# Optimization experiments

Hardware: AMD Instinct MI355X
Metric: run time of the kernel (lower is better)

The kernel has to match this reference:

```python
import jax, jax.numpy as jnp
import numpy as np

NUM_HEADS = 2

def mha(q, k, v, w_in, b_in, w_out, b_out):
    # torch nn.MultiheadAttention with batch_first=True, packed in_proj
    E = q.shape[-1]
    Dh = E // NUM_HEADS
    wq, wk, wv = jnp.split(w_in, 3, axis=0)
    bq, bk, bv = jnp.split(b_in, 3, axis=0)
    qh = (q @ wq.T + bq).reshape(q.shape[0], q.shape[1], NUM_HEADS, Dh)
    kh = (k @ wk.T + bk).reshape(k.shape[0], k.shape[1], NUM_HEADS, Dh)
    vh = (v @ wv.T + bv).reshape(v.shape[0], v.shape[1], NUM_HEADS, Dh)
    scores = jnp.einsum('blhd,bmhd->bhlm', qh, kh) / jnp.sqrt(jnp.asarray(Dh, q.dtype))
    attn = jax.nn.softmax(scores, axis=-1)
    ctx = jnp.einsum('bhlm,bmhd->blhd', attn, vh).reshape(q.shape[0], q.shape[1], E)
    return ctx @ w_out.T + b_out


def setup_inputs() -> dict:
    key = jax.random.key(0)
    ks = jax.random.split(key, 10)
    B, S, F, E, H = 16384, 512, 4, 8, 16
    s = 0.3
    return {
        'x': jax.random.normal(ks[0], (B, S, E), jnp.float32),
        'Q': jax.random.normal(ks[1], (F, E), jnp.float32) * s,
        'sa_w_in': jax.random.normal(ks[2], (3 * E, E), jnp.float32) * s,
        'sa_b_in': jnp.zeros((3 * E,), jnp.float32),
        'sa_w_out': jax.random.normal(ks[3], (E, E), jnp.float32) * s,
        'sa_b_out': jnp.zeros((E,), jnp.float32),
        'ca_w_in': jax.random.normal(ks[4], (3 * E, E), jnp.float32) * s,
        'ca_b_in': jnp.zeros((3 * E,), jnp.float32),
        'ca_w_out': jax.random.normal(ks[5], (E, E), jnp.float32) * s,
        'ca_b_out': jnp.zeros((E,), jnp.float32),
        'r_w1': jax.random.normal(ks[6], (H, F * E), jnp.float32) * s,
        'r_b1': jnp.zeros((H,), jnp.float32),
        'r_w2': jax.random.normal(ks[7], (1, H), jnp.float32) * s,
        'r_b2': jnp.zeros((1,), jnp.float32),
    }


def reference(x, Q, sa_w_in, sa_b_in, sa_w_out, sa_b_out,
              ca_w_in, ca_b_in, ca_w_out, ca_b_out,
              r_w1, r_b1, r_w2, r_b2):
    B = x.shape[0]
    # self-attention over the (batch-identical) factor queries
    Qb = jnp.broadcast_to(Q[None], (B,) + Q.shape)  # [B, F, E]
    Q_upd = mha(Qb, Qb, Qb, sa_w_in, sa_b_in, sa_w_out, sa_b_out)
    # cross-attention: factors attend over the input sequence
    Q_cross = mha(Q_upd, x, x, ca_w_in, ca_b_in, ca_w_out, ca_b_out)  # [B, F, E]
    similarity = jnp.einsum('bfe,bse->bfs', Q_cross, x)  # [B, F, S]
    attn_weights = jax.nn.softmax(similarity, axis=-1)
    final_factors = jnp.einsum('bfs,bse->bfe', attn_weights, x)  # [B, F, E]
    fused = final_factors.reshape(B, -1)  # [B, F*E]
    h = jax.nn.relu(fused @ r_w1.T + r_b1)
    out = h @ r_w2.T + r_b2  # [B, 1]
    return out, similarity
```

## Files before the change

### kernel.cpp

```cpp
#include <hip/hip_runtime.h>

#define SEQ 512
#define EMB 8
#define NFAC 4

__device__ __forceinline__ float rfl(float v) {
    return __int_as_float(__builtin_amdgcn_readfirstlane(__float_as_int(v)));
}

__global__ void precompute_kernel(
    const float* __restrict__ Q,
    const float* __restrict__ sa_w_in, const float* __restrict__ sa_b_in,
    const float* __restrict__ sa_w_out, const float* __restrict__ sa_b_out,
    const float* __restrict__ ca_w_in, const float* __restrict__ ca_b_in,
    const float* __restrict__ ca_w_out, const float* __restrict__ ca_b_out,
    float* __restrict__ ws)
{
    const int t = threadIdx.x;
    __shared__ float sw[608];
    __shared__ float sqh[32], skh[32], svh[32], sctx[32], sQu[32], sqc[32];
    enum { OQ = 0, SWIN = 32, SBIN = 224, SWOUT = 248, SBOUT = 312,
           CWIN = 320, CBIN = 512, CWOUT = 536, CBOUT = 600 };

    for (int i = t; i < 32;  i += 64) sw[OQ + i]    = Q[i];
    for (int i = t; i < 192; i += 64) sw[SWIN + i]  = sa_w_in[i];
    for (int i = t; i < 24;  i += 64) sw[SBIN + i]  = sa_b_in[i];
    for (int i = t; i < 64;  i += 64) sw[SWOUT + i] = sa_w_out[i];
    if (t < 8) sw[SBOUT + t] = sa_b_out[t];
    for (int i = t; i < 192; i += 64) sw[CWIN + i]  = ca_w_in[i];
    for (int i = t; i < 24;  i += 64) sw[CBIN + i]  = ca_b_in[i];
    for (int i = t; i < 64;  i += 64) sw[CWOUT + i] = ca_w_out[i];
    if (t < 8) sw[CBOUT + t] = ca_b_out[t];
    __syncthreads();

    {
        const int e2 = t >> 3, e = t & 7;
        float m0 = 0.f, m1 = 0.f;
        #pragma unroll
        for (int d = 0; d < 4; ++d) {
            m0 += sw[CWOUT + e2 * 8 + d]     * sw[CWIN + (16 + d) * 8 + e];
            m1 += sw[CWOUT + e2 * 8 + 4 + d] * sw[CWIN + (20 + d) * 8 + e];
        }
        ws[72 + t]  = m0;
        ws[136 + t] = m1;
    }
    if (t < 8) {
        float a = sw[CBOUT + t];
        #pragma unroll
        for (int d = 0; d < 8; ++d) a += sw[CWOUT + t * 8 + d] * sw[CBIN + 16 + d];
        ws[200 + t] = a;
    }

    if (t < 32) {
        const int l = t >> 3, j = t & 7;
        float aq = sw[SBIN + j], ak = sw[SBIN + 8 + j], av = sw[SBIN + 16 + j];
        #pragma unroll
        for (int e = 0; e < 8; ++e) {
            const float q = sw[OQ + l * 8 + e];
            aq += q * sw[SWIN + j * 8 + e];
            ak += q * sw[SWIN + (8 + j) * 8 + e];
            av += q * sw[SWIN + (16 + j) * 8 + e];
        }
        sqh[t] = aq; skh[t] = ak; svh[t] = av;
    }
    __syncthreads();

    if (t < 8) {
        const int h = t >> 2, l = t & 3;
        float sc[4], mx = -1e30f;
        #pragma unroll
        for (int m = 0; m < 4; ++m) {
            float a = 0.f;
            #pragma unroll
            for (int d = 0; d < 4; ++d) a += sqh[l * 8 + h * 4 + d] * skh[m * 8 + h * 4 + d];
            sc[m] = 0.5f * a;
            mx = fmaxf(mx, sc[m]);
        }
        float ssum = 0.f;
        #pragma unroll
        for (int m = 0; m < 4; ++m) { sc[m] = __expf(sc[m] - mx); ssum += sc[m]; }
        const float inv = 1.f / ssum;
        #pragma unroll
        for (int d = 0; d < 4; ++d) {
            float a = 0.f;
            #pragma unroll
            for (int m = 0; m < 4; ++m) a += sc[m] * svh[m * 8 + h * 4 + d];
            sctx[l * 8 + h * 4 + d] = a * inv;
        }
    }
    __syncthreads();

    if (t < 32) {
        const int l = t >> 3, e2 = t & 7;
        float a = sw[SBOUT + e2];
        #pragma unroll
        for (int e = 0; e < 8; ++e) a += sctx[l * 8 + e] * sw[SWOUT + e2 * 8 + e];
        sQu[l * 8 + e2] = a;
    }
    __syncthreads();

    if (t < 32) {
        const int l = t >> 3, j = t & 7;
        float a = sw[CBIN + j];
        #pragma unroll
        for (int e = 0; e < 8; ++e) a += sQu[l * 8 + e] * sw[CWIN + j * 8 + e];
        sqc[l * 8 + j] = a;
    }
    __syncthreads();

    {
        const int p = t >> 3, e = t & 7, h = p >> 2, f = p & 3;
        float a = 0.f;
        #pragma unroll
        for (int d = 0; d < 4; ++d)
            a += sqc[f * 8 + h * 4 + d] * sw[CWIN + (8 + h * 4 + d) * 8 + e];
        ws[p * 8 + e] = 0.5f * a;
    }
    if (t < 8) {
        const int p = t, h = p >> 2, f = p & 3;
        float a = 0.f;
        #pragma unroll
        for (int d = 0; d < 4; ++d) a += sqc[f * 8 + h * 4 + d] * sw[CBIN + 8 + h * 4 + d];
        ws[64 + p] = 0.5f * a;
    }
}

__global__ __launch_bounds__(256, 8) void fused_kernel(
    const float* __restrict__ x,
    const float* __restrict__ r_w1, const float* __restrict__ r_b1,
    const float* __restrict__ r_w2, const float* __restrict__ r_b2,
    const float* __restrict__ ws,
    float* __restrict__ out, float* __restrict__ sim_out)
{
    const int b = blockIdx.x;
    const int tid = threadIdx.x;
    const int w = __builtin_amdgcn_readfirstlane(tid >> 6);
    const int lane = tid & 63;
    const int c7 = lane & 7;

    __shared__ float su[64];
    __shared__ float sff[32];

    const float* xb = x + (size_t)b * (SEQ * EMB);

    const int p0 = 2 * w, p1 = 2 * w + 1;
    float wq0[8], wq1[8];
    #pragma unroll
    for (int e = 0; e < 8; ++e) {
        wq0[e] = rfl(ws[p0 * 8 + e]);
        wq1[e] = rfl(ws[p1 * 8 + e]);
    }
    const float cb0 = rfl(ws[64 + p0]), cb1 = rfl(ws[64 + p1]);

    float xa0[8] = {0.f,0.f,0.f,0.f,0.f,0.f,0.f,0.f};
    float xa1[8] = {0.f,0.f,0.f,0.f,0.f,0.f,0.f,0.f};
    float sum0 = 0.f, sum1 = 0.f;
    #pragma unroll
    for (int j = 0; j < 8; ++j) {
        const int s = lane + 64 * j;
        const float4* xp = (const float4*)(xb + s * 8);
        float4 lo = xp[0], hi = xp[1];
        float xv[8] = {lo.x, lo.y, lo.z, lo.w, hi.x, hi.y, hi.z, hi.w};
        float sc0 = cb0, sc1 = cb1;
        #pragma unroll
        for (int e = 0; e < 8; ++e) { sc0 += wq0[e] * xv[e]; sc1 += wq1[e] * xv[e]; }
        const float e0 = __expf(sc0), e1 = __expf(sc1);
        sum0 += e0; sum1 += e1;
        #pragma unroll
        for (int e = 0; e < 8; ++e) {
            xa0[e] += e0 * xv[e];
            xa1[e] += e1 * xv[e];
        }
    }
    #pragma unroll
    for (int m = 1; m < 8; m <<= 1) {
        sum0 += __shfl_xor(sum0, m, 64);
        sum1 += __shfl_xor(sum1, m, 64);
        #pragma unroll
        for (int e = 0; e < 8; ++e) {
            xa0[e] += __shfl_xor(xa0[e], m, 64);
            xa1[e] += __shfl_xor(xa1[e], m, 64);
        }
    }
    float v0 = xa0[0], v1 = xa1[0];
    #pragma unroll
    for (int e = 1; e < 8; ++e) {
        v0 = (c7 == e) ? xa0[e] : v0;
        v1 = (c7 == e) ? xa1[e] : v1;
    }
    #pragma unroll
    for (int m = 8; m < 64; m <<= 1) {
        sum0 += __shfl_xor(sum0, m, 64);
        sum1 += __shfl_xor(sum1, m, 64);
        v0 += __shfl_xor(v0, m, 64);
        v1 += __shfl_xor(v1, m, 64);
    }
    if (lane < 8) {
        su[p0 * 8 + lane] = v0 / sum0;
        su[p1 * 8 + lane] = v1 / sum1;
    }
    __syncthreads();

    float u0[8], u1[8];
    #pragma unroll
    for (int e = 0; e < 8; ++e) { u0[e] = su[w * 8 + e]; u1[e] = su[32 + w * 8 + e]; }
    float qv = ws[200 + c7];
    #pragma unroll
    for (int e = 0; e < 8; ++e)
        qv += ws[72 + c7 * 8 + e] * u0[e] + ws[136 + c7 * 8 + e] * u1[e];
    float qcr[8];
    #pragma unroll
    for (int e = 0; e < 8; ++e) qcr[e] = __shfl(qv, e, 64);

    float facc[8] = {0.f,0.f,0.f,0.f,0.f,0.f,0.f,0.f};
    float fsum = 0.f;
    float* simb = sim_out + (size_t)b * (NFAC * SEQ) + w * SEQ;
    #pragma unroll
    for (int j = 0; j < 8; ++j) {
        const int s = lane + 64 * j;
        const float4* xp = (const float4*)(xb + s * 8);
        float4 lo = xp[0], hi = xp[1];
        float xv[8] = {lo.x, lo.y, lo.z, lo.w, hi.x, hi.y, hi.z, hi.w};
        float sim = 0.f;
        #pragma unroll
        for (int e = 0; e < 8; ++e) sim += qcr[e] * xv[e];
        simb[s] = sim;
        const float ez = __expf(sim);
        fsum += ez;
        #pragma unroll
        for (int e = 0; e < 8; ++e) facc[e] += ez * xv[e];
    }
    #pragma unroll
    for (int m = 1; m < 8; m <<= 1) {
        fsum += __shfl_xor(fsum, m, 64);
        #pragma unroll
        for (int e = 0; e < 8; ++e) facc[e] += __shfl_xor(facc[e], m, 64);
    }
    float fv = facc[0];
    #pragma unroll
    for (int e = 1; e < 8; ++e) fv = (c7 == e) ? facc[e] : fv;
    #pragma unroll
    for (int m = 8; m < 64; m <<= 1) {
        fsum += __shfl_xor(fsum, m, 64);
        fv += __shfl_xor(fv, m, 64);
    }
    if (lane < 8) sff[w * 8 + lane] = fv / fsum;
    __syncthreads();

    if (tid < 16) {
        float a = r_b1[tid];
        const float4* w1p = (const float4*)(r_w1 + tid * 32);
        #pragma unroll
        for (int k = 0; k < 8; ++k) {
            float4 ww = w1p[k];
            a += ww.x * sff[4 * k + 0] + ww.y * sff[4 * k + 1]
               + ww.z * sff[4 * k + 2] + ww.w * sff[4 * k + 3];
        }
        a = fmaxf(a, 0.f);
        float v = a * r_w2[tid];
        v += __shfl_xor(v, 1, 64);
        v += __shfl_xor(v, 2, 64);
        v += __shfl_xor(v, 4, 64);
        v += __shfl_xor(v, 8, 64);
        if (tid == 0) out[b] = v + r_b2[0];
    }
}

extern "C" void kernel_launch(void* const* d_in, const int* in_sizes, int n_in,
                              void* d_out, int out_size, void* d_ws, size_t ws_size,
                              hipStream_t stream) {
    const float* x        = (const float*)d_in[0];
    const float* Q        = (const float*)d_in[1];
    const float* sa_w_in  = (const float*)d_in[2];
    const float* sa_b_in  = (const float*)d_in[3];
    const float* sa_w_out = (const float*)d_in[4];
    const float* sa_b_out = (const float*)d_in[5];
    const float* ca_w_in  = (const float*)d_in[6];
    const float* ca_b_in  = (const float*)d_in[7];
    const float* ca_w_out = (const float*)d_in[8];
    const float* ca_b_out = (const float*)d_in[9];
    const float* r_w1     = (const float*)d_in[10];
    const float* r_b1     = (const float*)d_in[11];
    const float* r_w2     = (const float*)d_in[12];
    const float* r_b2     = (const float*)d_in[13];

    float* out = (float*)d_out;
    const int B = in_sizes[0] / (SEQ * EMB);
    float* sim = out + B;
    float* ws  = (float*)d_ws;

    precompute_kernel<<<1, 64, 0, stream>>>(Q, sa_w_in, sa_b_in, sa_w_out, sa_b_out,
                                            ca_w_in, ca_b_in, ca_w_out, ca_b_out, ws);
    fused_kernel<<<B, 256, 0, stream>>>(x, r_w1, r_b1, r_w2, r_b2, ws, out, sim);
}
```

Measured before the change: 503.8 us.

## Keep x tile in registers across both passes and use packed float2 math

Each thread now loads its 8 rows of x into registers once and reuses them for both the cross-attention and the final similarity pass, instead of reading x from global memory twice. The dot products and accumulations are rewritten with 2-wide float vectors so the compiler can emit packed FP32 FMA instructions. Launch bounds are relaxed from 8 to 4 waves per SIMD to make room for the extra registers. This may lower occupancy and the ability to hide memory latency.

Measured after the change: 439.7 us. -12.7%, faster.

```diff
diff --git a/kernel.cpp b/kernel.cpp
--- a/kernel.cpp
+++ b/kernel.cpp
@@ -3,6 +3,8 @@
 #define SEQ 512
 #define EMB 8
 #define NFAC 4
+
+typedef float v2f __attribute__((ext_vector_type(2)));
 
 __device__ __forceinline__ float rfl(float v) {
     return __int_as_float(__builtin_amdgcn_readfirstlane(__float_as_int(v)));
@@ -125,7 +127,7 @@
     }
 }
 
-__global__ __launch_bounds__(256, 8) void fused_kernel(
+__global__ __launch_bounds__(256, 4) void fused_kernel(
     const float* __restrict__ x,
     const float* __restrict__ r_w1, const float* __restrict__ r_b1,
     const float* __restrict__ r_w2, const float* __restrict__ r_b2,
@@ -144,49 +146,54 @@
     const float* xb = x + (size_t)b * (SEQ * EMB);
 
     const int p0 = 2 * w, p1 = 2 * w + 1;
-    float wq0[8], wq1[8];
-    #pragma unroll
-    for (int e = 0; e < 8; ++e) {
-        wq0[e] = rfl(ws[p0 * 8 + e]);
-        wq1[e] = rfl(ws[p1 * 8 + e]);
+    v2f wq0[4], wq1[4];
+    #pragma unroll
+    for (int i = 0; i < 4; ++i) {
+        wq0[i] = v2f{rfl(ws[p0 * 8 + 2 * i]), rfl(ws[p0 * 8 + 2 * i + 1])};
+        wq1[i] = v2f{rfl(ws[p1 * 8 + 2 * i]), rfl(ws[p1 * 8 + 2 * i + 1])};
     }
     const float cb0 = rfl(ws[64 + p0]), cb1 = rfl(ws[64 + p1]);
 
-    float xa0[8] = {0.f,0.f,0.f,0.f,0.f,0.f,0.f,0.f};
-    float xa1[8] = {0.f,0.f,0.f,0.f,0.f,0.f,0.f,0.f};
+    float4 L0[8], L1[8];
+    #pragma unroll
+    for (int j = 0; j < 8; ++j) {
+        const float4* xp = (const float4*)(xb + (lane + 64 * j) * 8);
+        L0[j] = xp[0];
+        L1[j] = xp[1];
+    }
+
+    v2f xa0[4] = {}, xa1[4] = {};
     float sum0 = 0.f, sum1 = 0.f;
     #pragma unroll
     for (int j = 0; j < 8; ++j) {
-        const int s = lane + 64 * j;
-        const float4* xp = (const float4*)(xb + s * 8);
-        float4 lo = xp[0], hi = xp[1];
-        float xv[8] = {lo.x, lo.y, lo.z, lo.w, hi.x, hi.y, hi.z, hi.w};
-        float sc0 = cb0, sc1 = cb1;
-        #pragma unroll
-        for (int e = 0; e < 8; ++e) { sc0 += wq0[e] * xv[e]; sc1 += wq1[e] * xv[e]; }
-        const float e0 = __expf(sc0), e1 = __expf(sc1);
+        v2f xv[4];
+        xv[0] = v2f{L0[j].x, L0[j].y}; xv[1] = v2f{L0[j].z, L0[j].w};
+        xv[2] = v2f{L1[j].x, L1[j].y}; xv[3] = v2f{L1[j].z, L1[j].w};
+        v2f s0 = {cb0, 0.f}, s1 = {cb1, 0.f};
+        #pragma unroll
+        for (int i = 0; i < 4; ++i) { s0 += wq0[i] * xv[i]; s1 += wq1[i] * xv[i]; }
+        const float e0 = __expf(s0.x + s0.y), e1 = __expf(s1.x + s1.y);
         sum0 += e0; sum1 += e1;
         #pragma unroll
-        for (int e = 0; e < 8; ++e) {
-            xa0[e] += e0 * xv[e];
-            xa1[e] += e1 * xv[e];
-        }
-    }
+        for (int i = 0; i < 4; ++i) { xa0[i] += e0 * xv[i]; xa1[i] += e1 * xv[i]; }
+    }
+    float* a0 = (float*)xa0;
+    float* a1 = (float*)xa1;
     #pragma unroll
     for (int m = 1; m < 8; m <<= 1) {
         sum0 += __shfl_xor(sum0, m, 64);
         sum1 += __shfl_xor(sum1, m, 64);
         #pragma unroll
         for (int e = 0; e < 8; ++e) {
-            xa0[e] += __shfl_xor(xa0[e], m, 64);
-            xa1[e] += __shfl_xor(xa1[e], m, 64);
-        }
-    }
-    float v0 = xa0[0], v1 = xa1[0];
+            a0[e] += __shfl_xor(a0[e], m, 64);
+            a1[e] += __shfl_xor(a1[e], m, 64);
+        }
+    }
+    float v0 = a0[0], v1 = a1[0];
     #pragma unroll
     for (int e = 1; e < 8; ++e) {
-        v0 = (c7 == e) ? xa0[e] : v0;
-        v1 = (c7 == e) ? xa1[e] : v1;
+        v0 = (c7 == e) ? a0[e] : v0;
+        v1 = (c7 == e) ? a1[e] : v1;
     }
     #pragma unroll
     for (int m = 8; m < 64; m <<= 1) {
@@ -208,37 +215,40 @@
     #pragma unroll
     for (int e = 0; e < 8; ++e)
         qv += ws[72 + c7 * 8 + e] * u0[e] + ws[136 + c7 * 8 + e] * u1[e];
-    float qcr[8];
-    #pragma unroll
-    for (int e = 0; e < 8; ++e) qcr[e] = __shfl(qv, e, 64);
-
-    float facc[8] = {0.f,0.f,0.f,0.f,0.f,0.f,0.f,0.f};
+    v2f qcr[4];
+    #pragma unroll
+    for (int i = 0; i < 4; ++i)
+        qcr[i] = v2f{__shfl(qv, 2 * i, 64), __shfl(qv, 2 * i + 1, 64)};
+
+    v2f fac[4] = {};
     float fsum = 0.f;
     float* simb = sim_out + (size_t)b * (NFAC * SEQ) + w * SEQ;
     #pragma unroll
     for (int j = 0; j < 8; ++j) {
-        const int s = lane + 64 * j;
-        const float4* xp = (const float4*)(xb + s * 8);
-        float4 lo = xp[0], hi = xp[1];
-        float xv[8] = {lo.x, lo.y, lo.z, lo.w, hi.x, hi.y, hi.z, hi.w};
-        float sim = 0.f;
-        #pragma unroll
-        for (int e = 0; e < 8; ++e) sim += qcr[e] * xv[e];
-        simb[s] = sim;
+        v2f xv[4];
+        xv[0] = v2f{L0[j].x, L0[j].y}; xv[1] = v2f{L0[j].z, L0[j].w};
+        xv[2] = v2f{L1[j].x, L1[j].y}; xv[3] = v2f{L1[j].z, L1[j].w};
+        v2f sv = qcr[0] * xv[0];
+        sv += qcr[1] * xv[1];
+        sv += qcr[2] * xv[2];
+        sv += qcr[3] * xv[3];
+        const float sim = sv.x + sv.y;
+        simb[lane + 64 * j] = sim;
         const float ez = __expf(sim);
         fsum += ez;
         #pragma unroll
-        for (int e = 0; e < 8; ++e) facc[e] += ez * xv[e];
-    }
+        for (int i = 0; i < 4; ++i) fac[i] += ez * xv[i];
+    }
+    float* fa = (float*)fac;
     #pragma unroll
     for (int m = 1; m < 8; m <<= 1) {
         fsum += __shfl_xor(fsum, m, 64);
         #pragma unroll
-        for (int e = 0; e < 8; ++e) facc[e] += __shfl_xor(facc[e], m, 64);
-    }
-    float fv = facc[0];
-    #pragma unroll
-    for (int e = 1; e < 8; ++e) fv = (c7 == e) ? facc[e] : fv;
+        for (int e = 0; e < 8; ++e) fa[e] += __shfl_xor(fa[e], m, 64);
+    }
+    float fv = fa[0];
+    #pragma unroll
+    for (int e = 1; e < 8; ++e) fv = (c7 == e) ? fa[e] : fv;
     #pragma unroll
     for (int m = 8; m < 64; m <<= 1) {
         fsum += __shfl_xor(fsum, m, 64);
```
